# Optimization experiments

Measured on AMD Instinct MI355X. Metric: run time of the kernel, lower is better.

## Reference

```python
import jax, jax.numpy as jnp
import numpy as np

B, C, H, W = 64, 3, 224, 224
DEPTH = 2
NUM_OPS = 14

def _lin(m, lo, hi):
    return lo + m * (hi - lo)

def _clip255(x):
    return jnp.clip(x, 0.0, 255.0)

def _affine_sample(img, a, b, c, d, e, f):
    # img: [C,H,W]; inverse map (x_out,y_out)->(a*x+b*y+c, d*x+e*y+f); bilinear, zero fill.
    ch, h, w = img.shape
    ys, xs = jnp.meshgrid(jnp.arange(h, dtype=img.dtype), jnp.arange(w, dtype=img.dtype), indexing='ij')
    sx = a * xs + b * ys + c
    sy = d * xs + e * ys + f
    x0 = jnp.floor(sx); y0 = jnp.floor(sy)
    wx = sx - x0; wy = sy - y0
    def gather(yi, xi):
        valid = (xi >= 0) & (xi <= w - 1) & (yi >= 0) & (yi <= h - 1)
        v = img[:, jnp.clip(yi, 0, h - 1).astype(jnp.int32), jnp.clip(xi, 0, w - 1).astype(jnp.int32)]
        return jnp.where(valid[None], v, 0.0)
    v00 = gather(y0, x0); v01 = gather(y0, x0 + 1)
    v10 = gather(y0 + 1, x0); v11 = gather(y0 + 1, x0 + 1)
    top = v00 * (1 - wx) + v01 * wx
    bot = v10 * (1 - wx) + v11 * wx
    return top * (1 - wy) + bot * wy

def _gray(img):
    lum = jnp.array([0.299, 0.587, 0.114], img.dtype)
    return jnp.einsum('chw,c->hw', img, lum)

def shear_x(img, m):
    v = _lin(m, -0.3, 0.3)
    return _affine_sample(img, 1.0, v, 0.0, 0.0, 1.0, 0.0)

def shear_y(img, m):
    v = _lin(m, -0.3, 0.3)
    return _affine_sample(img, 1.0, 0.0, 0.0, v, 1.0, 0.0)

def translate_x(img, m):
    v = _lin(m, -0.45, 0.45) * img.shape[2]
    return _affine_sample(img, 1.0, 0.0, v, 0.0, 1.0, 0.0)

def translate_y(img, m):
    v = _lin(m, -0.45, 0.45) * img.shape[1]
    return _affine_sample(img, 1.0, 0.0, 0.0, 0.0, 1.0, v)

def rotate(img, m):
    rad = _lin(m, -30.0, 30.0) * np.pi / 180.0
    cx = (img.shape[2] - 1) * 0.5
    cy = (img.shape[1] - 1) * 0.5
    cs, sn = jnp.cos(rad), jnp.sin(rad)
    c = cx - cs * cx - sn * cy
    f = cy + sn * cx - cs * cy
    return _affine_sample(img, cs, sn, c, -sn, cs, f)

def brightness(img, m):
    return _clip255(img * _lin(m, 0.1, 1.9))

def color(img, m):
    g = _gray(img)[None]
    return _clip255(g + _lin(m, 0.1, 1.9) * (img - g))

def sharpness(img, m):
    k = jnp.array([[1., 1., 1.], [1., 5., 1.], [1., 1., 1.]], img.dtype) / 13.0
    ch = img.shape[0]
    kern = jnp.tile(k[None, None], (ch, 1, 1, 1))  # [C,1,3,3] depthwise
    blur = jax.lax.conv_general_dilated(img[None], kern, (1, 1), 'SAME', feature_group_count=ch)[0]
    out = _clip255(blur + _lin(m, 0.1, 1.9) * (img - blur))
    # PIL keeps the 1-px border unchanged
    out = out.at[:, 0, :].set(img[:, 0, :]).at[:, -1, :].set(img[:, -1, :])
    out = out.at[:, :, 0].set(img[:, :, 0]).at[:, :, -1].set(img[:, :, -1])
    return out

def contrast(img, m):
    mu = jnp.mean(_gray(img))
    return _clip255(mu + _lin(m, 0.1, 1.9) * (img - mu))

def solarize(img, m):
    thr = _lin(m, 0.0, 256.0)
    return jnp.where(img < thr, img, 255.0 - img)

def posterize(img, m):
    nbits = jnp.round(_lin(m, 0.0, 4.0))  # bits removed -> keep 8-nbits
    q = 2.0 ** nbits
    return jnp.floor(img / q) * q

def equalize(img, m):
    def eq_ch(chan):
        v = jnp.clip(jnp.round(chan), 0, 255).astype(jnp.int32)
        hist = jnp.zeros(256, jnp.int32).at[v.ravel()].add(1)
        step = (jnp.sum(hist) - hist[255]) // 255
        cum = jnp.concatenate([jnp.zeros(1, jnp.int32), jnp.cumsum(hist)[:-1]])
        lut = jnp.where(step > 0,
                        jnp.clip((cum + step // 2) // jnp.maximum(step, 1), 0, 255),
                        jnp.arange(256))
        return lut[v].astype(chan.dtype)
    return jax.vmap(eq_ch)(img)

def autocontrast(img, m):
    lo = jnp.min(img, axis=(1, 2), keepdims=True)
    hi = jnp.max(img, axis=(1, 2), keepdims=True)
    scale = 255.0 / jnp.maximum(hi - lo, 1e-6)
    return jnp.where(hi > lo, _clip255((img - lo) * scale), img)

def identity(img, m):
    return img

BRANCHES = [shear_x, shear_y, translate_x, translate_y, rotate, brightness, color,
            sharpness, contrast, solarize, posterize, equalize, autocontrast, identity]

def setup_inputs() -> dict:
    key = jax.random.key(0)
    k1, k2, k3, k4, k5 = jax.random.split(key, 5)
    x = jax.random.uniform(k1, (B, C, H, W), jnp.float32)          # [0,1]; module scales by 255
    ra_deform = jax.random.uniform(k2, (DEPTH, B), jnp.float32)    # magnitudes in [0,1]
    op_idx = jax.random.randint(k3, (DEPTH, B), 0, NUM_OPS, jnp.int32)
    p = jax.random.uniform(k4, (DEPTH, B), jnp.float32, 0.2, 0.8)  # p_min_t..p_max_t
    apply_mask = jax.random.uniform(k5, (DEPTH, B), jnp.float32) < p
    return {"x": x, "ra_deform": ra_deform, "op_idx": op_idx, "apply_mask": apply_mask}

def reference(x, ra_deform, op_idx, apply_mask):
    x = x * jnp.where(jnp.max(x) <= 1.0, 255.0, 1.0)
    x = x.astype(jnp.float32)
    def apply_one(img, j, m, ap):
        out = jax.lax.switch(j, BRANCHES, img, m)
        return jnp.where(ap, out, img)
    for i in range(DEPTH):  # small fixed depth
        x = jax.vmap(apply_one)(x, op_idx[i], ra_deform[i], apply_mask[i])
    return jnp.clip(x / 255.0, 0.0, 1.0)
```

## Files before the change

kernel.cpp:

```cpp
#include <hip/hip_runtime.h>

#define WID 224
#define HGT 224
#define HWp 50176
#define CHW 150528
#define NB  64
#define NSL 2048
#define SCH 1568
#define NT  9408
#define TPI 147
#define TPC 49

#define OFF_MAXB   0
#define OFF_HIST1  256
#define OFF_PSUM0  49408
#define OFF_PMIN0  51456
#define OFF_PMAX0  57600
#define OFF_PHIST0 63744
#define OFF_PSUM1  3209472
#define OFF_PMIN1  3247104
#define OFF_PMAX1  3284736
#define OFF_INTER  3322368

__device__ __forceinline__ float clip255(float v){ return fminf(fmaxf(v, 0.f), 255.f); }

__device__ __forceinline__ float wred(float v, int op){
    #pragma unroll
    for (int o = 32; o > 0; o >>= 1){
        float u = __shfl_down(v, o);
        v = (op==0) ? v+u : (op==1 ? fminf(v,u) : fmaxf(v,u));
    }
    return v;
}

__device__ __forceinline__ float blk_reduce(float v, float* red, int tid, int op){
    float w = wred(v, op);
    if ((tid & 63) == 0) red[tid >> 6] = w;
    __syncthreads();
    float a = red[0], b = red[1], c = red[2], d = red[3];
    float r = (op==0) ? (a+b)+(c+d) : (op==1 ? fminf(fminf(a,b),fminf(c,d)) : fmaxf(fmaxf(a,b),fmaxf(c,d)));
    __syncthreads();
    return r;
}

__device__ __forceinline__ const float* lut_scan(int hv, int* shh, float* slut, int tid, int* h255){
    if (tid == 255) *h255 = hv;
    shh[tid] = hv;
    __syncthreads();
    #pragma unroll
    for (int off = 1; off < 256; off <<= 1){
        int v = (tid >= off) ? shh[tid-off] : 0;
        __syncthreads();
        shh[tid] += v;
        __syncthreads();
    }
    int cum = shh[tid] - hv;
    int step = (HWp - *h255) / 255;
    int l = (step > 0) ? min(max((cum + (step >> 1)) / step, 0), 255) : tid;
    slut[tid] = (float)l;
    __syncthreads();
    return slut;
}

__device__ __forceinline__ float samp(const float* __restrict__ pl, float yi, float xi, float scl){
    if (xi < 0.f || xi > (float)(WID-1) || yi < 0.f || yi > (float)(HGT-1)) return 0.f;
    return pl[(int)yi * WID + (int)xi] * scl;
}

__device__ __forceinline__ void apply_body(const float* __restrict__ img,
                                           int c, int p, float4 v4,
                                           int j, int ap, float m, float scl,
                                           float mu, float lo, float hi,
                                           const float* lut,
                                           float o[4])
{
    int y = p / WID;
    int x = p - y*WID;
    const float* pl = img + c*HWp;
    float vr[4] = {v4.x, v4.y, v4.z, v4.w};
    float iv[4] = {v4.x*scl, v4.y*scl, v4.z*scl, v4.w*scl};

    if (!ap) {
        #pragma unroll
        for (int k = 0; k < 4; k++) o[k] = iv[k];
        return;
    }
    switch (j){
    case 0: case 2: {
        float off = (j==0) ? (-0.3f + 0.6f*m)*(float)y
                           : (-0.45f + 0.9f*m)*(float)WID;
        float sx0 = (float)x + off;
        float x0f = floorf(sx0);
        float wx  = sx0 - x0f;
        int   x0  = (int)x0f;
        const float* row = pl + y*WID;
        float v[5];
        #pragma unroll
        for (int k = 0; k < 5; k++){
            int col = x0 + k;
            v[k] = (col >= 0 && col < WID) ? row[col]*scl : 0.f;
        }
        #pragma unroll
        for (int k = 0; k < 4; k++) o[k] = v[k]*(1.f-wx) + v[k+1]*wx;
        break; }
    case 3: {
        float ff  = (-0.45f + 0.9f*m)*(float)HGT;
        float sy0 = (float)y + ff;
        float y0f = floorf(sy0);
        float wy  = sy0 - y0f;
        int   y0  = (int)y0f;
        float4 t4 = {0.f,0.f,0.f,0.f}, b4 = {0.f,0.f,0.f,0.f};
        if (y0   >= 0 && y0   < HGT) t4 = *(const float4*)(pl + y0*WID + x);
        if (y0+1 >= 0 && y0+1 < HGT) b4 = *(const float4*)(pl + (y0+1)*WID + x);
        float tt[4] = {t4.x,t4.y,t4.z,t4.w}, bb[4] = {b4.x,b4.y,b4.z,b4.w};
        #pragma unroll
        for (int k = 0; k < 4; k++) o[k] = (tt[k]*scl)*(1.f-wy) + (bb[k]*scl)*wy;
        break; }
    case 1: {
        float dd = -0.3f + 0.6f*m;
        #pragma unroll
        for (int k = 0; k < 4; k++){
            float sy = dd*(float)(x+k) + (float)y;
            float y0f = floorf(sy);
            float wy  = sy - y0f;
            int   y0  = (int)y0f;
            int col = x + k;
            float tv = (y0   >= 0 && y0   < HGT) ? pl[y0*WID + col]*scl : 0.f;
            float bv = (y0+1 >= 0 && y0+1 < HGT) ? pl[(y0+1)*WID + col]*scl : 0.f;
            o[k] = tv*(1.f-wy) + bv*wy;
        }
        break; }
    case 4: {
        float deg = -30.f + 60.f*m;
        float rad = deg * (float)(3.14159265358979323846/180.0);
        float cs = cosf(rad), sn = sinf(rad);
        float cx = (WID-1)*0.5f, cy = (HGT-1)*0.5f;
        float a = cs, bb = sn, dd = -sn, ee = cs;
        float cc = cx - cs*cx - sn*cy;
        float ff = cy + sn*cx - cs*cy;
        float yf = (float)y;
        #pragma unroll
        for (int k = 0; k < 4; k++){
            float xf = (float)(x + k);
            float sx = a*xf + bb*yf + cc;
            float sy = dd*xf + ee*yf + ff;
            float x0f = floorf(sx), y0f = floorf(sy);
            float wx = sx - x0f, wy = sy - y0f;
            float v00 = samp(pl, y0f,     x0f,     scl);
            float v01 = samp(pl, y0f,     x0f+1.f, scl);
            float v10 = samp(pl, y0f+1.f, x0f,     scl);
            float v11 = samp(pl, y0f+1.f, x0f+1.f, scl);
            float top = v00*(1.f-wx) + v01*wx;
            float bot = v10*(1.f-wx) + v11*wx;
            o[k] = top*(1.f-wy) + bot*wy;
        }
        break; }
    case 5: {
        float f = 0.1f + 1.8f*m;
        #pragma unroll
        for (int k = 0; k < 4; k++) o[k] = clip255(iv[k]*f);
        break; }
    case 6: {
        float4 r4 = *(const float4*)(img + p);
        float4 g4 = *(const float4*)(img + HWp + p);
        float4 b4 = *(const float4*)(img + 2*HWp + p);
        float rr[4] = {r4.x*scl, r4.y*scl, r4.z*scl, r4.w*scl};
        float gg[4] = {g4.x*scl, g4.y*scl, g4.z*scl, g4.w*scl};
        float bl[4] = {b4.x*scl, b4.y*scl, b4.z*scl, b4.w*scl};
        float f = 0.1f + 1.8f*m;
        #pragma unroll
        for (int k = 0; k < 4; k++){
            float g = 0.299f*rr[k] + 0.587f*gg[k] + 0.114f*bl[k];
            o[k] = clip255(g + f*(iv[k] - g));
        }
        break; }
    case 7: {
        float f = 0.1f + 1.8f*m;
        if (y == 0 || y == HGT-1){
            #pragma unroll
            for (int k = 0; k < 4; k++) o[k] = iv[k];
        } else {
            float4 up4 = *(const float4*)(pl + p - WID);
            float4 dn4 = *(const float4*)(pl + p + WID);
            bool hasL = (x > 0), hasR = (x < WID-4);
            float u0 = hasL ? pl[p-WID-1] : 0.f, u5 = hasR ? pl[p-WID+4] : 0.f;
            float c0 = hasL ? pl[p-1]     : 0.f, c5 = hasR ? pl[p+4]     : 0.f;
            float d0 = hasL ? pl[p+WID-1] : 0.f, d5 = hasR ? pl[p+WID+4] : 0.f;
            float uu[6] = {u0, up4.x, up4.y, up4.z, up4.w, u5};
            float cc[6] = {c0, vr[0], vr[1], vr[2], vr[3], c5};
            float dd[6] = {d0, dn4.x, dn4.y, dn4.z, dn4.w, d5};
            #pragma unroll
            for (int k = 0; k < 4; k++){
                int xx = x + k;
                if (xx == 0 || xx == WID-1) o[k] = iv[k];
                else {
                    float s8 = uu[k]+uu[k+1]+uu[k+2] + cc[k]+cc[k+2] + dd[k]+dd[k+1]+dd[k+2];
                    float blur = (s8*scl + 5.f*iv[k]) * (1.f/13.f);
                    o[k] = clip255(blur + f*(iv[k] - blur));
                }
            }
        }
        break; }
    case 8: {
        float f = 0.1f + 1.8f*m;
        #pragma unroll
        for (int k = 0; k < 4; k++) o[k] = clip255(mu + f*(iv[k] - mu));
        break; }
    case 9: {
        float thr = 256.f*m;
        #pragma unroll
        for (int k = 0; k < 4; k++) o[k] = (iv[k] < thr) ? iv[k] : 255.f - iv[k];
        break; }
    case 10: {
        float q = exp2f(rintf(4.f*m));
        #pragma unroll
        for (int k = 0; k < 4; k++) o[k] = floorf(iv[k]/q)*q;
        break; }
    case 11: {
        #pragma unroll
        for (int k = 0; k < 4; k++){
            int ivi = min(max((int)rintf(iv[k]), 0), 255);
            o[k] = lut[ivi];
        }
        break; }
    case 12: {
        float sc = 255.f / fmaxf(hi - lo, 1e-6f);
        #pragma unroll
        for (int k = 0; k < 4; k++)
            o[k] = (hi > lo) ? clip255((iv[k] - lo) * sc) : iv[k];
        break; }
    default:
        #pragma unroll
        for (int k = 0; k < 4; k++) o[k] = iv[k];
        break;
    }
}

__global__ void k1_stats(const float* __restrict__ x, const int* __restrict__ op,
                         const int* __restrict__ mask, float* __restrict__ wsf)
{
    __shared__ float red[4];
    __shared__ int sh[1536];
    int* ints = (int*)wsf;
    float* psum0 = wsf + OFF_PSUM0;
    float* pmin0 = wsf + OFF_PMIN0;
    float* pmax0 = wsf + OFF_PMAX0;
    int* phist0 = (int*)wsf + OFF_PHIST0;
    int* hist1  = (int*)wsf + OFF_HIST1;

    int blk = blockIdx.x, tid = threadIdx.x;
    if (tid < 24) hist1[blk*24 + tid] = 0;

    int b = blk >> 5, s = blk & 31;
    int j = op[b], ap = mask[b];
    bool needSum  = ap && (j == 8);
    bool needMM   = ap && (j == 12);
    bool needHist = ap && (j == 11);
    const float* img = x + (size_t)b * CHW;
    int p0 = s * SCH;
    const float GW[3] = {0.299f, 0.587f, 0.114f};

    float mx = 0.f, gs = 0.f;
    for (int c = 0; c < 3; c++){
        const float* pl = img + c*HWp + p0;
        float lo = 3.4e38f, hi = 0.f, cs = 0.f;
        for (int p = tid*4; p < SCH; p += 1024){
            float4 v = *(const float4*)(pl + p);
            float m4 = fmaxf(fmaxf(v.x, v.y), fmaxf(v.z, v.w));
            mx = fmaxf(mx, m4);
            if (needMM){ hi = fmaxf(hi, m4); lo = fminf(lo, fminf(fminf(v.x,v.y), fminf(v.z,v.w))); }
            if (needSum) cs += (v.x + v.y) + (v.z + v.w);
        }
        if (needSum) gs += GW[c] * cs;
        if (needMM){
            float l = blk_reduce(lo, red, tid, 1);
            if (!tid) pmin0[blk*3 + c] = l;
            float h = blk_reduce(hi, red, tid, 2);
            if (!tid) pmax0[blk*3 + c] = h;
        }
    }
    float bm = blk_reduce(mx, red, tid, 2);
    if (!tid) atomicMax(&ints[OFF_MAXB], __float_as_int(bm));
    if (needSum){
        float t = blk_reduce(gs, red, tid, 0);
        if (!tid) psum0[blk] = t;
    }
    if (needHist){
        for (int i = tid; i < 1536; i += 256) sh[i] = 0;
        __syncthreads();
        for (int c = 0; c < 3; c++){
            const float* pl = img + c*HWp + p0;
            for (int p = tid; p < SCH; p += 256){
                float v = pl[p];
                atomicAdd(&sh[c*256 + min(max((int)rintf(v), 0), 255)], 1);
                atomicAdd(&sh[768 + c*256 + min(max((int)rintf(v*255.f), 0), 255)], 1);
            }
        }
        __syncthreads();
        for (int i = tid; i < 1536; i += 256) phist0[blk*1536 + i] = sh[i];
    }
}

__global__ void k2_apply0(const float* __restrict__ x, const float* __restrict__ ra,
                          const int* __restrict__ op, const int* __restrict__ mask,
                          float* __restrict__ wsf)
{
    __shared__ float red[4];
    __shared__ int   shh[256];
    __shared__ float slut[256];
    __shared__ int   h255;
    const int* ints = (const int*)wsf;
    const float* psum0 = wsf + OFF_PSUM0;
    const float* pmin0 = wsf + OFF_PMIN0;
    const float* pmax0 = wsf + OFF_PMAX0;
    const int* phist0 = (const int*)wsf + OFF_PHIST0;
    int* hist1 = (int*)wsf + OFF_HIST1;
    float* psum1 = wsf + OFF_PSUM1;
    float* pmin1 = wsf + OFF_PMIN1;
    float* pmax1 = wsf + OFF_PMAX1;
    float* inter = wsf + OFF_INTER;

    int t = blockIdx.x, tid = threadIdx.x;
    int b = t / TPI;
    int r = t - b*TPI;
    int c = r / TPC;
    int p = (r - c*TPC)*1024 + tid*4;

    const float* img = x + (size_t)b*CHW;
    float4 v4 = *(const float4*)(img + c*HWp + p);

    float scl = (__int_as_float(ints[OFF_MAXB]) <= 1.0f) ? 255.f : 1.f;
    int j = op[b], ap = mask[b];
    float m = ra[b];

    float mu = 0.f, lo = 0.f, hi = 0.f;
    const float* lut = nullptr;
    if (ap){
        if (j == 8){
            float v = (tid < 32) ? psum0[b*32 + tid] : 0.f;
            mu = blk_reduce(v, red, tid, 0) * scl * (1.f/(float)HWp);
        } else if (j == 12){
            float v  = (tid < 32) ? pmin0[(b*32 + tid)*3 + c] : 3.4e38f;
            lo = blk_reduce(v, red, tid, 1) * scl;
            float v2 = (tid < 32) ? pmax0[(b*32 + tid)*3 + c] : 0.f;
            hi = blk_reduce(v2, red, tid, 2) * scl;
        } else if (j == 11){
            int d = (scl == 255.f) ? 1 : 0;
            const int* ph = phist0 + d*768 + c*256 + tid;
            int sum = 0;
            #pragma unroll 8
            for (int s = 0; s < 32; s++) sum += ph[(b*32 + s)*1536];
            lut = lut_scan(sum, shh, slut, tid, &h255);
        }
    }

    float o[4];
    apply_body(img, c, p, v4, j, ap, m, scl, mu, lo, hi, lut, o);
    float4 w = {o[0], o[1], o[2], o[3]};
    *(float4*)(inter + (size_t)b*CHW + c*HWp + p) = w;

    int j1 = op[NB + b], ap1 = mask[NB + b];
    if (ap1 && (j1 == 8 || j1 == 11 || j1 == 12)){
        const float GW[3] = {0.299f, 0.587f, 0.114f};
        int wv = tid >> 6;
        if (j1 == 8){
            float s4 = (o[0] + o[1]) + (o[2] + o[3]);
            float ws = wred(s4, 0);
            if ((tid & 63) == 0) psum1[t*4 + wv] = ws * GW[c];
        } else if (j1 == 12){
            float l4 = fminf(fminf(o[0],o[1]), fminf(o[2],o[3]));
            float h4 = fmaxf(fmaxf(o[0],o[1]), fmaxf(o[2],o[3]));
            float wl = wred(l4, 1);
            float wh = wred(h4, 2);
            if ((tid & 63) == 0){ pmin1[t*4 + wv] = wl; pmax1[t*4 + wv] = wh; }
        } else {
            __syncthreads();
            shh[tid] = 0;
            __syncthreads();
            #pragma unroll
            for (int k = 0; k < 4; k++)
                atomicAdd(&shh[min(max((int)rintf(o[k]), 0), 255)], 1);
            __syncthreads();
            int v = shh[tid];
            if (v) atomicAdd(&hist1[b*768 + c*256 + tid], v);
        }
    }
}

__global__ void k3_apply1(const float* __restrict__ ra, const int* __restrict__ op,
                          const int* __restrict__ mask, float* __restrict__ out,
                          float* __restrict__ wsf)
{
    __shared__ float red[4];
    __shared__ int   shh[256];
    __shared__ float slut[256];
    __shared__ int   h255;
    const int* hist1 = (const int*)wsf + OFF_HIST1;
    const float* psum1 = wsf + OFF_PSUM1;
    const float* pmin1 = wsf + OFF_PMIN1;
    const float* pmax1 = wsf + OFF_PMAX1;
    const float* inter = wsf + OFF_INTER;

    int t = blockIdx.x, tid = threadIdx.x;
    int b = t / TPI;
    int r = t - b*TPI;
    int c = r / TPC;
    int p = (r - c*TPC)*1024 + tid*4;

    const float* img = inter + (size_t)b*CHW;
    float4 v4 = *(const float4*)(img + c*HWp + p);

    int j = op[NB + b], ap = mask[NB + b];
    float m = ra[NB + b];

    float mu = 0.f, lo = 0.f, hi = 0.f;
    const float* lut = nullptr;
    if (ap){
        if (j == 8){
            float v = 0.f;
            for (int i = tid; i < TPI*4; i += 256) v += psum1[b*TPI*4 + i];
            mu = blk_reduce(v, red, tid, 0) * (1.f/(float)HWp);
        } else if (j == 12){
            float v  = (tid < TPC*4) ? pmin1[(b*TPI + c*TPC)*4 + tid] : 3.4e38f;
            lo = blk_reduce(v, red, tid, 1);
            float v2 = (tid < TPC*4) ? pmax1[(b*TPI + c*TPC)*4 + tid] : 0.f;
            hi = blk_reduce(v2, red, tid, 2);
        } else if (j == 11){
            lut = lut_scan(hist1[b*768 + c*256 + tid], shh, slut, tid, &h255);
        }
    }

    float o[4];
    apply_body(img, c, p, v4, j, ap, m, 1.f, mu, lo, hi, lut, o);
    float4 w;
    w.x = fminf(fmaxf(o[0]*(1.f/255.f), 0.f), 1.f);
    w.y = fminf(fmaxf(o[1]*(1.f/255.f), 0.f), 1.f);
    w.z = fminf(fmaxf(o[2]*(1.f/255.f), 0.f), 1.f);
    w.w = fminf(fmaxf(o[3]*(1.f/255.f), 0.f), 1.f);
    *(float4*)(out + (size_t)b*CHW + c*HWp + p) = w;
}

extern "C" void kernel_launch(void* const* d_in, const int* in_sizes, int n_in,
                              void* d_out, int out_size, void* d_ws, size_t ws_size,
                              hipStream_t stream) {
    const float* x    = (const float*)d_in[0];
    const float* ra   = (const float*)d_in[1];
    const int*   op   = (const int*)d_in[2];
    const int*   mask = (const int*)d_in[3];
    float* out = (float*)d_out;
    float* wsf = (float*)d_ws;

    k1_stats <<<NSL, 256, 0, stream>>>(x, op, mask, wsf);
    k2_apply0<<<NT,  256, 0, stream>>>(x, ra, op, mask, wsf);
    k3_apply1<<<NT,  256, 0, stream>>>(ra, op, mask, out, wsf);
}
```

Measured before the change: 145.1 us.

## Process two float4 chunks per thread and fuse histogram into stats pass

The apply kernels now have each block cover 2048 pixels instead of 1024, which halves the grid and amortises the per-block stat reductions and LUT scans over twice the work. The last tile in each channel is half-full and is guarded. The stats kernel now builds its histogram inside the main float4 pass, so the plane is no longer read a second time. A fast in-bounds path skips per-element bounds checks for horizontal shifts. Larger blocks reduce the number of waves available for latency hiding, and the 2048-pixel partial sums now feed the psum1/pmin1 layouts.

```diff
diff --git a/kernel.cpp b/kernel.cpp
--- a/kernel.cpp
+++ b/kernel.cpp
@@ -7,9 +7,9 @@
 #define NB  64
 #define NSL 2048
 #define SCH 1568
-#define NT  9408
-#define TPI 147
-#define TPC 49
+#define TPI2 75
+#define TPC2 25
+#define NT2 4800
 
 #define OFF_MAXB   0
 #define OFF_HIST1  256
@@ -95,10 +95,15 @@
         int   x0  = (int)x0f;
         const float* row = pl + y*WID;
         float v[5];
-        #pragma unroll
-        for (int k = 0; k < 5; k++){
-            int col = x0 + k;
-            v[k] = (col >= 0 && col < WID) ? row[col]*scl : 0.f;
+        if (x0 >= 0 && x0 <= WID-5){
+            #pragma unroll
+            for (int k = 0; k < 5; k++) v[k] = row[x0+k]*scl;
+        } else {
+            #pragma unroll
+            for (int k = 0; k < 5; k++){
+                int col = x0 + k;
+                v[k] = (col >= 0 && col < WID) ? row[col]*scl : 0.f;
+            }
         }
         #pragma unroll
         for (int k = 0; k < 4; k++) o[k] = v[k]*(1.f-wx) + v[k+1]*wx;
@@ -260,6 +265,11 @@
     int p0 = s * SCH;
     const float GW[3] = {0.299f, 0.587f, 0.114f};
 
+    if (needHist){
+        for (int i = tid; i < 1536; i += 256) sh[i] = 0;
+        __syncthreads();
+    }
+
     float mx = 0.f, gs = 0.f;
     for (int c = 0; c < 3; c++){
         const float* pl = img + c*HWp + p0;
@@ -270,6 +280,14 @@
             mx = fmaxf(mx, m4);
             if (needMM){ hi = fmaxf(hi, m4); lo = fminf(lo, fminf(fminf(v.x,v.y), fminf(v.z,v.w))); }
             if (needSum) cs += (v.x + v.y) + (v.z + v.w);
+            if (needHist){
+                float vv[4] = {v.x, v.y, v.z, v.w};
+                #pragma unroll
+                for (int k = 0; k < 4; k++){
+                    atomicAdd(&sh[c*256 + min(max((int)rintf(vv[k]), 0), 255)], 1);
+                    atomicAdd(&sh[768 + c*256 + min(max((int)rintf(vv[k]*255.f), 0), 255)], 1);
+                }
+            }
         }
         if (needSum) gs += GW[c] * cs;
         if (needMM){
@@ -286,16 +304,6 @@
         if (!tid) psum0[blk] = t;
     }
     if (needHist){
-        for (int i = tid; i < 1536; i += 256) sh[i] = 0;
-        __syncthreads();
-        for (int c = 0; c < 3; c++){
-            const float* pl = img + c*HWp + p0;
-            for (int p = tid; p < SCH; p += 256){
-                float v = pl[p];
-                atomicAdd(&sh[c*256 + min(max((int)rintf(v), 0), 255)], 1);
-                atomicAdd(&sh[768 + c*256 + min(max((int)rintf(v*255.f), 0), 255)], 1);
-            }
-        }
         __syncthreads();
         for (int i = tid; i < 1536; i += 256) phist0[blk*1536 + i] = sh[i];
     }
@@ -321,13 +329,18 @@
     float* inter = wsf + OFF_INTER;
 
     int t = blockIdx.x, tid = threadIdx.x;
-    int b = t / TPI;
-    int r = t - b*TPI;
-    int c = r / TPC;
-    int p = (r - c*TPC)*1024 + tid*4;
+    int b = t / TPI2;
+    int r = t - b*TPI2;
+    int c = r / TPC2;
+    int q = r - c*TPC2;
+    int p  = q*2048 + tid*4;
+    int p2 = p + 1024;
+    bool full = (q < TPC2-1);
 
     const float* img = x + (size_t)b*CHW;
-    float4 v4 = *(const float4*)(img + c*HWp + p);
+    const float* pl  = img + c*HWp;
+    float4 va = *(const float4*)(pl + p);
+    float4 vb = full ? *(const float4*)(pl + p2) : make_float4(0.f,0.f,0.f,0.f);
 
     float scl = (__int_as_float(ints[OFF_MAXB]) <= 1.0f) ? 255.f : 1.f;
     int j = op[b], ap = mask[b];
@@ -354,24 +367,31 @@
         }
     }
 
-    float o[4];
-    apply_body(img, c, p, v4, j, ap, m, scl, mu, lo, hi, lut, o);
-    float4 w = {o[0], o[1], o[2], o[3]};
-    *(float4*)(inter + (size_t)b*CHW + c*HWp + p) = w;
+    float oa[4], ob[4] = {0.f,0.f,0.f,0.f};
+    apply_body(img, c, p, va, j, ap, m, scl, mu, lo, hi, lut, oa);
+    if (full) apply_body(img, c, p2, vb, j, ap, m, scl, mu, lo, hi, lut, ob);
+    float* dst = inter + (size_t)b*CHW + c*HWp;
+    *(float4*)(dst + p) = make_float4(oa[0], oa[1], oa[2], oa[3]);
+    if (full) *(float4*)(dst + p2) = make_float4(ob[0], ob[1], ob[2], ob[3]);
 
     int j1 = op[NB + b], ap1 = mask[NB + b];
     if (ap1 && (j1 == 8 || j1 == 11 || j1 == 12)){
         const float GW[3] = {0.299f, 0.587f, 0.114f};
         int wv = tid >> 6;
         if (j1 == 8){
-            float s4 = (o[0] + o[1]) + (o[2] + o[3]);
-            float ws = wred(s4, 0);
+            float s8 = (oa[0]+oa[1])+(oa[2]+oa[3]);
+            if (full) s8 += (ob[0]+ob[1])+(ob[2]+ob[3]);
+            float ws = wred(s8, 0);
             if ((tid & 63) == 0) psum1[t*4 + wv] = ws * GW[c];
         } else if (j1 == 12){
-            float l4 = fminf(fminf(o[0],o[1]), fminf(o[2],o[3]));
-            float h4 = fmaxf(fmaxf(o[0],o[1]), fmaxf(o[2],o[3]));
-            float wl = wred(l4, 1);
-            float wh = wred(h4, 2);
+            float l8 = fminf(fminf(oa[0],oa[1]), fminf(oa[2],oa[3]));
+            float h8 = fmaxf(fmaxf(oa[0],oa[1]), fmaxf(oa[2],oa[3]));
+            if (full){
+                l8 = fminf(l8, fminf(fminf(ob[0],ob[1]), fminf(ob[2],ob[3])));
+                h8 = fmaxf(h8, fmaxf(fmaxf(ob[0],ob[1]), fmaxf(ob[2],ob[3])));
+            }
+            float wl = wred(l8, 1);
+            float wh = wred(h8, 2);
             if ((tid & 63) == 0){ pmin1[t*4 + wv] = wl; pmax1[t*4 + wv] = wh; }
         } else {
             __syncthreads();
@@ -379,7 +399,12 @@
             __syncthreads();
             #pragma unroll
             for (int k = 0; k < 4; k++)
-                atomicAdd(&shh[min(max((int)rintf(o[k]), 0), 255)], 1);
+                atomicAdd(&shh[min(max((int)rintf(oa[k]), 0), 255)], 1);
+            if (full){
+                #pragma unroll
+                for (int k = 0; k < 4; k++)
+                    atomicAdd(&shh[min(max((int)rintf(ob[k]), 0), 255)], 1);
+            }
             __syncthreads();
             int v = shh[tid];
             if (v) atomicAdd(&hist1[b*768 + c*256 + tid], v);
@@ -402,13 +427,18 @@
     const float* inter = wsf + OFF_INTER;
 
     int t = blockIdx.x, tid = threadIdx.x;
-    int b = t / TPI;
-    int r = t - b*TPI;
-    int c = r / TPC;
-    int p = (r - c*TPC)*1024 + tid*4;
+    int b = t / TPI2;
+    int r = t - b*TPI2;
+    int c = r / TPC2;
+    int q = r - c*TPC2;
+    int p  = q*2048 + tid*4;
+    int p2 = p + 1024;
+    bool full = (q < TPC2-1);
 
     const float* img = inter + (size_t)b*CHW;
-    float4 v4 = *(const float4*)(img + c*HWp + p);
+    const float* pl  = img + c*HWp;
+    float4 va = *(const float4*)(pl + p);
+    float4 vb = full ? *(const float4*)(pl + p2) : make_float4(0.f,0.f,0.f,0.f);
 
     int j = op[NB + b], ap = mask[NB + b];
     float m = ra[NB + b];
@@ -418,26 +448,37 @@
     if (ap){
         if (j == 8){
             float v = 0.f;
-            for (int i = tid; i < TPI*4; i += 256) v += psum1[b*TPI*4 + i];
+            for (int i = tid; i < TPI2*4; i += 256) v += psum1[b*TPI2*4 + i];
             mu = blk_reduce(v, red, tid, 0) * (1.f/(float)HWp);
         } else if (j == 12){
-            float v  = (tid < TPC*4) ? pmin1[(b*TPI + c*TPC)*4 + tid] : 3.4e38f;
+            float v  = (tid < TPC2*4) ? pmin1[(b*TPI2 + c*TPC2)*4 + tid] : 3.4e38f;
             lo = blk_reduce(v, red, tid, 1);
-            float v2 = (tid < TPC*4) ? pmax1[(b*TPI + c*TPC)*4 + tid] : 0.f;
+            float v2 = (tid < TPC2*4) ? pmax1[(b*TPI2 + c*TPC2)*4 + tid] : 0.f;
             hi = blk_reduce(v2, red, tid, 2);
         } else if (j == 11){
             lut = lut_scan(hist1[b*768 + c*256 + tid], shh, slut, tid, &h255);
         }
     }
 
-    float o[4];
-    apply_body(img, c, p, v4, j, ap, m, 1.f, mu, lo, hi, lut, o);
+    float oa[4], ob[4];
+    apply_body(img, c, p, va, j, ap, m, 1.f, mu, lo, hi, lut, oa);
+    if (full) apply_body(img, c, p2, vb, j, ap, m, 1.f, mu, lo, hi, lut, ob);
+
+    float* dst = out + (size_t)b*CHW + c*HWp;
     float4 w;
-    w.x = fminf(fmaxf(o[0]*(1.f/255.f), 0.f), 1.f);
-    w.y = fminf(fmaxf(o[1]*(1.f/255.f), 0.f), 1.f);
-    w.z = fminf(fmaxf(o[2]*(1.f/255.f), 0.f), 1.f);
-    w.w = fminf(fmaxf(o[3]*(1.f/255.f), 0.f), 1.f);
-    *(float4*)(out + (size_t)b*CHW + c*HWp + p) = w;
+    w.x = fminf(fmaxf(oa[0]*(1.f/255.f), 0.f), 1.f);
+    w.y = fminf(fmaxf(oa[1]*(1.f/255.f), 0.f), 1.f);
+    w.z = fminf(fmaxf(oa[2]*(1.f/255.f), 0.f), 1.f);
+    w.w = fminf(fmaxf(oa[3]*(1.f/255.f), 0.f), 1.f);
+    *(float4*)(dst + p) = w;
+    if (full){
+        float4 w2;
+        w2.x = fminf(fmaxf(ob[0]*(1.f/255.f), 0.f), 1.f);
+        w2.y = fminf(fmaxf(ob[1]*(1.f/255.f), 0.f), 1.f);
+        w2.z = fminf(fmaxf(ob[2]*(1.f/255.f), 0.f), 1.f);
+        w2.w = fminf(fmaxf(ob[3]*(1.f/255.f), 0.f), 1.f);
+        *(float4*)(dst + p2) = w2;
+    }
 }
 
 extern "C" void kernel_launch(void* const* d_in, const int* in_sizes, int n_in,
@@ -451,6 +492,6 @@
     float* wsf = (float*)d_ws;
 
     k1_stats <<<NSL, 256, 0, stream>>>(x, op, mask, wsf);
-    k2_apply0<<<NT,  256, 0, stream>>>(x, ra, op, mask, wsf);
-    k3_apply1<<<NT,  256, 0, stream>>>(ra, op, mask, out, wsf);
-}
+    k2_apply0<<<NT2, 256, 0, stream>>>(x, ra, op, mask, wsf);
+    k3_apply1<<<NT2, 256, 0, stream>>>(ra, op, mask, out, wsf);
+}
```

After: 143.6 us. About the same (-1.0%).
